# Optimization experiments

Measured on AMD Instinct MI355X. Metric: run time of the kernel, lower is better.

Reference implementation:

```python
import jax, jax.numpy as jnp
import numpy as np

# Detect.__init__ defaults from the source
TOP_K = 5000
CONF_THRESH = 0.01
NMS_THRESH = 0.3
VAR0, VAR1 = 0.1, 0.2   # variance = [0.1, 0.2]
NUM_CLASSES = 2

B = 16
IMAGE = 1280
FMAPS = [320, 160, 80, 40, 20, 10]          # image / steps [4,8,16,32,64,128]
MIN_SIZES = [16, 32, 64, 128, 256, 512]
AR = 1.5                                     # aspect_ratios = [[1.5]] * 6


def make_priors():
    """Vectorized PriorBox.forward: 1 prior per location (max_sizes=[], single AR)."""
    chunks = []
    for f, ms in zip(FMAPS, MIN_SIZES):
        c = (np.arange(f, dtype=np.float32) + 0.5) / f
        cy, cx = np.meshgrid(c, c, indexing='ij')
        s = ms / float(IMAGE)
        w = np.full_like(cx, s / np.sqrt(AR))   # s_k / sqrt(ar)
        h = np.full_like(cx, s * np.sqrt(AR))   # s_k * sqrt(ar)
        chunks.append(np.stack([cx, cy, w, h], -1).reshape(-1, 4))
    pr = np.concatenate(chunks, 0).clip(0.0, 1.0)   # clip=True
    return jnp.asarray(pr, jnp.float32)             # [136500, 4]


def setup_inputs() -> dict:
    key = jax.random.key(0)
    k1, k2 = jax.random.split(key)
    P = sum(f * f for f in FMAPS)   # 136500
    loc_data = 0.5 * jax.random.normal(k1, (B, P, 4), jnp.float32)
    conf_data = jax.random.uniform(k2, (B * P, NUM_CLASSES), jnp.float32)  # post-softmax probs
    prior_data = make_priors()
    return {"loc_data": loc_data, "conf_data": conf_data, "prior_data": prior_data}


def _decode(loc, priors):
    # SSD box decode with variances [0.1, 0.2]; loc, priors: [P,4]
    cxcy = priors[:, :2] + loc[:, :2] * VAR0 * priors[:, 2:]
    wh = priors[:, 2:] * jnp.exp(loc[:, 2:] * VAR1)
    xy1 = cxcy - wh * 0.5
    xy2 = xy1 + wh
    return jnp.concatenate([xy1, xy2], axis=-1)   # [P,4] x1y1x2y2


def _greedy_keep(boxes, valid):
    # Greedy NMS over score-sorted candidates. boxes [K,4], valid [K] bool.
    # Indices/keep decisions are discrete -> computed on stop_gradient'd boxes.
    b = jax.lax.stop_gradient(boxes)
    x1, y1, x2, y2 = b[:, 0], b[:, 1], b[:, 2], b[:, 3]
    area = (x2 - x1) * (y2 - y1)
    idxs = jnp.arange(b.shape[0])

    def body(keep, i):
        iw = jnp.maximum(jnp.minimum(x2, x2[i]) - jnp.maximum(x1, x1[i]), 0.0)
        ih = jnp.maximum(jnp.minimum(y2, y2[i]) - jnp.maximum(y1, y1[i]), 0.0)
        inter = iw * ih
        iou = inter / (area + area[i] - inter)
        suppress = keep[i] & (iou > NMS_THRESH) & (idxs > i)
        return keep & ~suppress, None

    keep, _ = jax.lax.scan(body, valid, idxs)
    return keep


def _detect_one(loc_i, conf_cl, priors):
    # loc_i [P,4]; conf_cl [P] = class-1 scores; returns [TOP_K, 5] (score, x1,y1,x2,y2)
    boxes = _decode(loc_i, priors)
    masked = jnp.where(conf_cl > CONF_THRESH, conf_cl, -1.0)   # c_mask gating
    order = jnp.argsort(-jax.lax.stop_gradient(masked))[:TOP_K]  # scores.sort, top_k cap
    s = masked[order]
    b = boxes[order]
    valid = s > CONF_THRESH
    keep = _greedy_keep(b, valid)
    # scatter kept (score, box) rows, in descending-score order, into dense output
    rank = jnp.cumsum(keep) - 1
    row = jnp.where(keep, rank, TOP_K)            # dropped rows -> scratch slot
    vals = jnp.concatenate([s[:, None], b], axis=1)
    vals = jnp.where(keep[:, None], vals, 0.0)
    out = jnp.zeros((TOP_K + 1, 5), jnp.float32).at[row].set(vals)
    return out[:TOP_K]


def reference(loc_data, conf_data, prior_data):
    num = loc_data.shape[0]
    P = prior_data.shape[0]
    conf_preds = conf_data.reshape(num, P, NUM_CLASSES).transpose(0, 2, 1)  # [B,2,P]
    cls1 = jax.vmap(_detect_one, in_axes=(0, 0, None))(loc_data, conf_preds[:, 1, :], prior_data)
    bg = jnp.zeros_like(cls1)                     # background class row stays zero
    output = jnp.stack([bg, cls1], axis=1)        # [B, 2, TOP_K, 5]
    # NOTE: the original's final `flt[(rank < top_k)...].fill_(0)` fills a boolean-indexed
    # COPY in torch, so it is a no-op on `output`; we faithfully return output unchanged.
    return output
```

## Files before the change

kernel.cpp:

```cpp
#include <hip/hip_runtime.h>
#include <math.h>

#pragma clang fp contract(off)

#define PNUM 136500
#define HPNUM 68250
#define BNUM 16
#define TOPK 5000
#define CAP 8192
#define NB4 4096
#define WBASE 0x2F000u
#define GCS 4
#define NWORDS 79
#define NW32 158
#define GSTRIDE 32
#define CAPE 65536
#define ELDS 14336
#define NXB 128
#define NWC 8
#define NXB2 1024
#define BSTRIDE 5120
#define EBUF 3072
#define SLOTS 4
#define SKI(i) ((i) + ((i) >> 4))

#define OFF_SC    ((size_t)0)
#define OFF_BOX4  (OFF_SC + 320000)
#define OFF_HIST  (OFF_BOX4 + 1280000)
#define OFF_GBCUR (OFF_HIST + 262144)
#define OFF_ECNT  (OFF_GBCUR + 1048576)
#define OFF_BCNT  (OFF_ECNT + 2048)
#define OFF_BCUR  (OFF_BCNT + 65536)
#define OFF_WCNT  (OFF_BCUR + 65536)
#define OFF_ZEND  (OFF_WCNT + 64)
#define OFF_CUT   (OFF_ZEND)
#define OFF_SBASE (OFF_CUT + 64)
#define OFF_WL    (OFF_SBASE + 262144)
#define OFF_KEYS  (OFF_WL + 262144)
#define OFF_EDGE  (OFF_KEYS + 1048576)
#define OFF_GRP   (OFF_EDGE + 4194304)
#define OFF_BOFS  (OFF_GRP)
#define OFF_SIDX  (OFF_GRP + 16384)
#define OFF_SBOX  (OFF_SIDX + 327680)

__device__ __forceinline__ unsigned f2ord(float f) {
    unsigned u = __float_as_uint(f);
    return (u & 0x80000000u) ? ~u : (u | 0x80000000u);
}
__device__ __forceinline__ float ord2f(unsigned o) {
    unsigned u = (o & 0x80000000u) ? (o ^ 0x80000000u) : ~o;
    return __uint_as_float(u);
}
__device__ __forceinline__ int bucketOf(float x) {
    int b = (int)((x + 0.6f) * 71.111115f);
    return (b < 0) ? 0 : ((b > 127) ? 127 : b);
}
__device__ __forceinline__ int rkeyOf(float x1, float x2) {
    int b = bucketOf(x1);
    int wc = bucketOf(x2) - b;
    if (wc > NWC - 1) wc = NWC - 1;
    if (wc < 0) wc = 0;
    return b * NWC + wc;
}

__global__ void __launch_bounds__(512) k_hist(const float* __restrict__ conf,
                                              unsigned* __restrict__ hist) {
    __shared__ unsigned lh[NB4];
    int img = blockIdx.y;
    for (int i = threadIdx.x; i < NB4; i += 512) lh[i] = 0;
    __syncthreads();
    const float4* src = (const float4*)(conf + (size_t)img * PNUM * 2);
    int stride = gridDim.x * 512;
    for (int q = blockIdx.x * 512 + threadIdx.x; q < HPNUM; q += stride) {
        float4 v = src[q];
        if (v.y > 0.01f) atomicAdd(&lh[(f2ord(v.y) >> 14) - WBASE], 1u);
        if (v.w > 0.01f) atomicAdd(&lh[(f2ord(v.w) >> 14) - WBASE], 1u);
    }
    __syncthreads();
    unsigned* h = hist + (size_t)img * NB4;
    for (int i = threadIdx.x; i < NB4; i += 512) {
        unsigned c = lh[i];
        if (c) atomicAdd(&h[i], c);
    }
}

__global__ void __launch_bounds__(256) k_cutoff2(const unsigned* __restrict__ hist,
                                                 unsigned* __restrict__ cut,
                                                 unsigned* __restrict__ sbase,
                                                 unsigned* __restrict__ wl,
                                                 unsigned* __restrict__ wcnt) {
    __shared__ unsigned csum[256], suf[256], scut;
    int img = blockIdx.x;
    int t = threadIdx.x;
    const unsigned* h = hist + (size_t)img * NB4;
    unsigned hv[16];
    unsigned s = 0;
    #pragma unroll
    for (int j = 0; j < 16; ++j) { hv[j] = h[t * 16 + j]; s += hv[j]; }
    csum[t] = s;
    __syncthreads();
    if (t == 0) {
        unsigned a = 0;
        for (int g = 255; g >= 0; --g) { unsigned c = csum[g]; suf[g] = a; a += c; }
        unsigned acc = 0, before = 0;
        int c = -1;
        for (int cc = 255; cc >= 0; --cc) {
            if (acc + csum[cc] >= (unsigned)TOPK) { c = cc; before = acc; break; }
            acc += csum[cc];
        }
        unsigned cutb = WBASE;
        if (c >= 0) {
            unsigned s2 = before;
            cutb = WBASE + (unsigned)c * 16u;
            for (int b = c * 16 + 15; b >= c * 16; --b) {
                s2 += h[b];
                if (s2 >= (unsigned)TOPK) { cutb = WBASE + (unsigned)b; break; }
            }
        }
        scut = cutb;
        cut[img] = cutb;
    }
    __syncthreads();
    unsigned cutb = scut;
    unsigned acc = suf[t];
    unsigned* sb = sbase + (size_t)img * NB4 + t * 16;
    sb[15] = acc;
    #pragma unroll
    for (int j = 14; j >= 0; --j) { acc += hv[j + 1]; sb[j] = acc; }
    #pragma unroll
    for (int j = 0; j < 16; ++j) {
        unsigned b = (unsigned)t * 16u + (unsigned)j;
        if (WBASE + b >= cutb && hv[j] > 0) {
            unsigned x = atomicAdd(wcnt, 1u);
            wl[x] = ((unsigned)img << 12) | b;
        }
    }
}

__global__ void __launch_bounds__(256) k_gather2(
        const float* __restrict__ conf, const unsigned* __restrict__ cut,
        const unsigned* __restrict__ sbase, unsigned* __restrict__ gbcur,
        unsigned long long* __restrict__ keys) {
    int q = blockIdx.x * 256 + threadIdx.x;
    int img = blockIdx.y;
    if (q >= HPNUM) return;
    unsigned cutb = cut[img];
    float4 v = ((const float4*)(conf + (size_t)img * PNUM * 2))[q];
    const unsigned* sb = sbase + (size_t)img * NB4;
    unsigned* gc = gbcur + (size_t)img * NB4 * GCS;
    unsigned long long* kp = keys + (size_t)img * CAP;
    #pragma unroll
    for (int e = 0; e < 2; ++e) {
        float s = e ? v.w : v.y;
        if (s > 0.01f) {
            unsigned o = f2ord(s);
            unsigned w18 = o >> 14;
            if (w18 >= cutb) {
                unsigned wb = w18 - WBASE;
                unsigned pos = sb[wb] + atomicAdd(&gc[wb * GCS], 1u);
                if (pos < (unsigned)CAP)
                    kp[pos] = ((unsigned long long)o << 32)
                              | (unsigned)(~(unsigned)(2 * q + e));
            }
        }
    }
}

__global__ void __launch_bounds__(256) k_ssortdec(
        const unsigned long long* __restrict__ keys,
        const unsigned* __restrict__ hist, const unsigned* __restrict__ sbase,
        const unsigned* __restrict__ wl, const unsigned* __restrict__ wcnt,
        const float* __restrict__ loc, const float* __restrict__ pri,
        float* __restrict__ SC, float4* __restrict__ BOX4,
        unsigned* __restrict__ bcnt) {
    __shared__ unsigned long long sk[1088];
    __shared__ unsigned lhist[NXB2];
    int tid = threadIdx.x;
    unsigned nW = *wcnt;
    for (unsigned w = blockIdx.x; w < nW; w += gridDim.x) {
        unsigned ent = wl[w];
        int img = (int)(ent >> 12);
        int b = (int)(ent & 4095u);
        unsigned cnt = hist[(size_t)img * NB4 + b];
        unsigned base = sbase[(size_t)img * NB4 + b];
        if (base >= (unsigned)TOPK) continue;
        const unsigned long long* kp = keys + (size_t)img * CAP + base;
        for (int i = tid; i < NXB2; i += 256) lhist[i] = 0;
        unsigned scnt = cnt > 1024 ? 1024u : cnt;
        if (scnt >= 2) {
            unsigned np2 = 2;
            while (np2 < scnt) np2 <<= 1;
            for (unsigned i = tid; i < np2; i += 256)
                sk[SKI(i)] = (i < scnt) ? kp[i] : 0ull;
            __syncthreads();
            for (unsigned k = 2; k <= np2; k <<= 1) {
                for (unsigned j = k >> 1; j > 0; j >>= 1) {
                    for (unsigned t = tid; t < (np2 >> 1); t += 256) {
                        unsigned i = ((t & ~(j - 1)) << 1) | (t & (j - 1));
                        unsigned p = i | j;
                        bool desc = ((i & k) == 0);
                        unsigned long long a = sk[SKI(i)], bb = sk[SKI(p)];
                        bool sw = desc ? (a < bb) : (a > bb);
                        if (sw) { sk[SKI(i)] = bb; sk[SKI(p)] = a; }
                    }
                    __syncthreads();
                }
            }
        } else {
            if (tid == 0 && scnt == 1) sk[0] = kp[0];
            __syncthreads();
        }
        size_t ibase = (size_t)img * TOPK;
        for (unsigned i = tid; i < cnt; i += 256) {
            unsigned r = base + i;
            if (r >= (unsigned)TOPK) continue;
            unsigned long long key = (i < scnt) ? sk[SKI(i)] : kp[i];
            float s, x1, y1, x2, y2;
            if (key != 0ull) {
                unsigned ordv = (unsigned)(key >> 32);
                s = ord2f(ordv);
                unsigned p = ~(unsigned)(key & 0xFFFFFFFFull);
                const float* lp = loc + ((size_t)img * PNUM + p) * 4;
                const float* pp = pri + (size_t)p * 4;
                float lx = lp[0], ly = lp[1], lw = lp[2], lh = lp[3];
                float px = pp[0], py = pp[1], pw = pp[2], ph = pp[3];
                float cx = px + (lx * 0.1f) * pw;
                float cy = py + (ly * 0.1f) * ph;
                float w2 = pw * expf(lw * 0.2f);
                float h2 = ph * expf(lh * 0.2f);
                x1 = cx - w2 * 0.5f;
                y1 = cy - h2 * 0.5f;
                x2 = x1 + w2;
                y2 = y1 + h2;
            } else {
                s = -1.0f; x1 = 0.f; y1 = 0.f; x2 = 0.f; y2 = 0.f;
            }
            SC[ibase + r] = s;
            BOX4[ibase + r] = make_float4(x1, y1, x2, y2);
            atomicAdd(&lhist[rkeyOf(x1, x2)], 1u);
        }
        __syncthreads();
        for (int i = tid; i < NXB2; i += 256) {
            unsigned c = lhist[i];
            if (c) atomicAdd(&bcnt[img * NXB2 + i], c);
        }
        __syncthreads();
    }
}

__global__ void __launch_bounds__(256) k_bscat(
        const unsigned* __restrict__ bcnt, unsigned* __restrict__ bcur,
        const float4* __restrict__ BOX4,
        unsigned* __restrict__ bofs, unsigned* __restrict__ sidx,
        float4* __restrict__ sbox, float* __restrict__ out) {
    __shared__ unsigned bpre[NXB2 + 1], tsum[256];
    int img = blockIdx.y;
    int tid = threadIdx.x;
    uint4* oz = (uint4*)(out + (size_t)img * 2 * TOPK * 5);
    uint4 z4 = make_uint4(0u, 0u, 0u, 0u);
    for (int i = blockIdx.x * 256 + tid; i < 12500; i += 20 * 256) oz[i] = z4;
    const unsigned* bc = bcnt + img * NXB2;
    unsigned l0 = bc[tid * 4], l1 = bc[tid * 4 + 1],
             l2 = bc[tid * 4 + 2], l3 = bc[tid * 4 + 3];
    tsum[tid] = l0 + l1 + l2 + l3;
    __syncthreads();
    if (tid == 0) {
        unsigned a = 0;
        for (int t = 0; t < 256; ++t) { unsigned c = tsum[t]; tsum[t] = a; a += c; }
        bpre[NXB2] = a;
    }
    __syncthreads();
    unsigned a = tsum[tid];
    bpre[tid * 4] = a;
    bpre[tid * 4 + 1] = a + l0;
    bpre[tid * 4 + 2] = a + l0 + l1;
    bpre[tid * 4 + 3] = a + l0 + l1 + l2;
    __syncthreads();
    if (blockIdx.x == 0) {
        if (tid < NXB) bofs[img * 130 + tid] = bpre[tid * NWC];
        if (tid == 0) bofs[img * 130 + NXB] = bpre[NXB2];
    }
    int r = blockIdx.x * 256 + tid;
    if (r < TOPK) {
        float4 b = BOX4[(size_t)img * TOPK + r];
        int bk = rkeyOf(b.x, b.z);
        unsigned sp = bpre[bk] + atomicAdd(&bcur[img * NXB2 + bk], 1u);
        int base = img * BSTRIDE;
        sidx[base + sp] = (unsigned)r;
        sbox[base + sp] = b;
    }
}

__global__ void __launch_bounds__(256) k_pair4(
        const unsigned* __restrict__ bofs, const unsigned* __restrict__ sidx,
        const float4* __restrict__ sbox,
        unsigned* __restrict__ ecnt, unsigned* __restrict__ edges) {
    __shared__ unsigned ebuf[EBUF];
    __shared__ unsigned ecl, ebase;
    int img = blockIdx.y;
    int wid = threadIdx.x >> 6;
    int lane = threadIdx.x & 63;
    int sb0 = (blockIdx.x * 4 + wid) * SLOTS;
    if (threadIdx.x == 0) ecl = 0;
    __syncthreads();
    unsigned* ec = ecnt + (size_t)img * GSTRIDE;
    unsigned* eg = edges + (size_t)img * CAPE;
    if (sb0 < TOPK) {
        int base = img * BSTRIDE;
        float x1k[SLOTS], x2k[SLOTS], y1k[SLOTS], y2k[SLOTS], ark[SLOTS];
        unsigned rk[SLOTS];
        bool act[SLOTS];
        #pragma unroll
        for (int k = 0; k < SLOTS; ++k) {
            act[k] = (sb0 + k) < TOPK;
            int s = act[k] ? (sb0 + k) : sb0;
            float4 bk = sbox[base + s];
            x1k[k] = bk.x; y1k[k] = bk.y; x2k[k] = bk.z; y2k[k] = bk.w;
            ark[k] = (bk.z - bk.x) * (bk.w - bk.y);
            rk[k] = sidx[base + s];
        }
        int b1 = bucketOf(x1k[0]);
        int b2m = bucketOf(x2k[0]);
        float gymin = y1k[0], gymax = y2k[0];
        #pragma unroll
        for (int k = 1; k < SLOTS; ++k)
            if (act[k]) {
                int b = bucketOf(x2k[k]); if (b > b2m) b2m = b;
                gymin = fminf(gymin, y1k[k]);
                gymax = fmaxf(gymax, y2k[k]);
            }
        const unsigned* bo = bofs + img * 130;
        unsigned s0 = bo[b1], s1 = bo[b2m + 1];
        if (s0 < s1) {
            unsigned nit = (s1 - s0 + 63) >> 6;
            unsigned c0 = s0 + (unsigned)lane;
            if (c0 > s1 - 1) c0 = s1 - 1;
            float4 cb = sbox[base + c0];
            unsigned cr = sidx[base + c0];
            for (unsigned it = 0; it < nit; ++it) {
                float4 nb = cb; unsigned nr = cr;
                if (it + 1 < nit) {
                    unsigned cn = s0 + (it + 1) * 64 + (unsigned)lane;
                    if (cn > s1 - 1) cn = s1 - 1;
                    nb = sbox[base + cn];
                    nr = sidx[base + cn];
                }
                bool in = (s0 + it * 64 + (unsigned)lane) < s1;
                bool yok = in && (cb.w > gymin) && (cb.y < gymax);
                float bar = (cb.z - cb.x) * (cb.w - cb.y);
                #pragma unroll
                for (int k = 0; k < SLOTS; ++k) {
                    bool hit = false;
                    unsigned edge = 0;
                    if (yok && act[k] && cb.x >= x1k[k]
                        && !(cb.x == x1k[k] && cr <= rk[k])) {
                        float dx = fminf(x2k[k], cb.z) - fmaxf(x1k[k], cb.x);
                        if (dx > 0.0f) {
                            float dy = fminf(y2k[k], cb.w) - fmaxf(y1k[k], cb.y);
                            if (dy > 0.0f) {
                                float inter = dx * dy;
                                float iou = inter / (bar + ark[k] - inter);
                                if (iou > 0.3f) {
                                    unsigned su = (rk[k] < cr) ? rk[k] : cr;
                                    unsigned vi = (rk[k] < cr) ? cr : rk[k];
                                    edge = (vi << 13) | su;
                                    hit = true;
                                }
                            }
                        }
                    }
                    unsigned long long bal = __ballot(hit);
                    if (bal) {
                        int n = __popcll(bal);
                        unsigned wb = 0;
                        if (lane == 0) wb = atomicAdd(&ecl, (unsigned)n);
                        wb = __shfl(wb, 0, 64);
                        if (hit) {
                            unsigned long long lt =
                                (lane == 0) ? 0ull : ((1ull << lane) - 1ull);
                            unsigned p = wb + (unsigned)__popcll(bal & lt);
                            if (p < (unsigned)EBUF) ebuf[p] = edge;
                            else {
                                unsigned gp = atomicAdd(ec, 1u);
                                if (gp < (unsigned)CAPE) eg[gp] = edge;
                            }
                        }
                    }
                }
                cb = nb; cr = nr;
            }
        }
    }
    __syncthreads();
    unsigned n = min(ecl, (unsigned)EBUF);
    if (threadIdx.x == 0 && n) ebase = atomicAdd(ec, n);
    __syncthreads();
    for (unsigned i = threadIdx.x; i < n; i += 256) {
        unsigned p = ebase + i;
        if (p < (unsigned)CAPE) eg[p] = ebuf[i];
    }
}

__global__ void __launch_bounds__(256) k_nms3(
        const float* __restrict__ SC, const float4* __restrict__ BOX4,
        const unsigned* __restrict__ ecnt, const unsigned* __restrict__ edges,
        float* __restrict__ out) {
    __shared__ unsigned lgrp[ELDS];
    __shared__ unsigned undL[160], keptL[160], blockL[160];
    __shared__ unsigned pfx[80];
    __shared__ int chg[2];
    int img = blockIdx.x;
    int tid = threadIdx.x;
    int l = tid & 63;
    int wid = tid >> 6;
    size_t ib = (size_t)img * TOPK;
    const float* sc = SC + ib;

    if (tid < 160) { keptL[tid] = 0u; blockL[tid] = 0u; }
    if (tid < 2) chg[tid] = 0;
    for (int w = wid; w < NWORDS; w += 4) {
        int row = w * 64 + l;
        bool valid = (row < TOPK) && (sc[row] > 0.01f);
        unsigned long long b = __ballot(valid);
        if (l == 0) {
            undL[2 * w]     = (unsigned)b;
            undL[2 * w + 1] = (unsigned)(b >> 32);
        }
    }
    unsigned E = min(ecnt[(size_t)img * GSTRIDE], (unsigned)CAPE);
    const unsigned* eimg = edges + (size_t)img * CAPE;
    bool inl = (E <= (unsigned)ELDS);
    if (inl) for (unsigned e = tid; e < E; e += 256) lgrp[e] = eimg[e];
    __syncthreads();

    for (int round = 0; round < 256; ++round) {
        int par = round & 1;
        for (unsigned e = tid; e < E; e += 256) {
            unsigned ed = inl ? lgrp[e] : eimg[e];
            unsigned s = ed & 8191u;
            unsigned v = ed >> 13;
            unsigned sw = s >> 5, sb = s & 31u;
            unsigned vw = v >> 5, vb = 1u << (v & 31u);
            if ((keptL[sw] >> sb) & 1u) {
                if (undL[vw] & vb) {
                    unsigned old = atomicAnd(&undL[vw], ~vb);
                    if (old & vb) chg[par] = 1;
                }
            } else if ((undL[sw] >> sb) & 1u) {
                if (!(blockL[vw] & vb)) atomicOr(&blockL[vw], vb);
            }
        }
        __syncthreads();
        if (tid < NW32) {
            unsigned nk = undL[tid] & ~blockL[tid];
            if (nk) {
                keptL[tid] |= nk;
                undL[tid] &= ~nk;
                chg[par] = 1;
            }
            blockL[tid] = 0u;
        }
        if (tid == 0) chg[par ^ 1] = 0;
        __syncthreads();
        if (!chg[par]) break;
    }

    if (tid == 0) {
        unsigned acc = 0;
        for (int w = 0; w < NWORDS; ++w) {
            pfx[w] = acc;
            acc += (unsigned)(__popc(keptL[2 * w]) + __popc(keptL[2 * w + 1]));
        }
    }
    __syncthreads();
    const float4* bx = BOX4 + ib;
    float* op = out + (((size_t)img * 2) + 1) * TOPK * 5;
    for (int w = wid; w < NWORDS; w += 4) {
        unsigned long long kw =
            ((unsigned long long)keptL[2 * w + 1] << 32) | keptL[2 * w];
        if (!kw) continue;
        int row = w * 64 + l;
        if ((kw >> l) & 1ull) {
            int rank = (int)pfx[w] + (int)__popcll(kw & ((1ull << l) - 1ull));
            float4 b = bx[row];
            float* r = op + (size_t)rank * 5;
            r[0] = sc[row]; r[1] = b.x; r[2] = b.y; r[3] = b.z; r[4] = b.w;
        }
    }
}

extern "C" void kernel_launch(void* const* d_in, const int* in_sizes, int n_in,
                              void* d_out, int out_size, void* d_ws, size_t ws_size,
                              hipStream_t stream) {
    (void)in_sizes; (void)n_in; (void)ws_size; (void)out_size;
    const float* loc  = (const float*)d_in[0];
    const float* conf = (const float*)d_in[1];
    const float* pri  = (const float*)d_in[2];
    float* out = (float*)d_out;
    char* ws = (char*)d_ws;

    float* SC   = (float*)(ws + OFF_SC);
    float4* BOX4 = (float4*)(ws + OFF_BOX4);
    unsigned* hist = (unsigned*)(ws + OFF_HIST);
    unsigned* cut  = (unsigned*)(ws + OFF_CUT);
    unsigned* sbase = (unsigned*)(ws + OFF_SBASE);
    unsigned* gbcur = (unsigned*)(ws + OFF_GBCUR);
    unsigned long long* keys = (unsigned long long*)(ws + OFF_KEYS);
    unsigned* ecnt = (unsigned*)(ws + OFF_ECNT);
    unsigned* bcnt = (unsigned*)(ws + OFF_BCNT);
    unsigned* bcur = (unsigned*)(ws + OFF_BCUR);
    unsigned* wcnt = (unsigned*)(ws + OFF_WCNT);
    unsigned* wl   = (unsigned*)(ws + OFF_WL);
    unsigned* edges = (unsigned*)(ws + OFF_EDGE);
    unsigned* bofs = (unsigned*)(ws + OFF_BOFS);
    unsigned* sidx = (unsigned*)(ws + OFF_SIDX);
    float4* sbox = (float4*)(ws + OFF_SBOX);

    hipMemsetAsync(ws + OFF_HIST, 0, OFF_ZEND - OFF_HIST, stream);

    dim3 gh1(16, BNUM);
    k_hist<<<gh1, 512, 0, stream>>>(conf, hist);
    k_cutoff2<<<BNUM, 256, 0, stream>>>(hist, cut, sbase, wl, wcnt);
    dim3 gh2((HPNUM + 255) / 256, BNUM);
    k_gather2<<<gh2, 256, 0, stream>>>(conf, cut, sbase, gbcur, keys);
    k_ssortdec<<<1024, 256, 0, stream>>>(keys, hist, sbase, wl, wcnt,
                                         loc, pri, SC, BOX4, bcnt);
    dim3 gb((TOPK + 255) / 256, BNUM);
    k_bscat<<<gb, 256, 0, stream>>>(bcnt, bcur, BOX4, bofs, sidx, sbox, out);
    dim3 pg((TOPK + 4 * SLOTS - 1) / (4 * SLOTS), BNUM);
    k_pair4<<<pg, 256, 0, stream>>>(bofs, sidx, sbox, ecnt, edges);
    k_nms3<<<BNUM, 256, 0, stream>>>(SC, BOX4, ecnt, edges, out);
}
```

Measured before the change: 212.1 us.

## Fuse all detection stages into one cooperative persistent kernel with grid syncs

```diff
diff --git a/kernel.cpp b/kernel.cpp
--- a/kernel.cpp
+++ b/kernel.cpp
@@ -1,7 +1,10 @@
 #include <hip/hip_runtime.h>
+#include <hip/hip_cooperative_groups.h>
 #include <math.h>
 
 #pragma clang fp contract(off)
+
+namespace cg = cooperative_groups;
 
 #define PNUM 136500
 #define HPNUM 68250
@@ -23,6 +26,9 @@
 #define EBUF 3072
 #define SLOTS 4
 #define SKI(i) ((i) + ((i) >> 4))
+#define NVB_G 267
+#define NVB_P 313
+#define NVB_B 20
 
 #define OFF_SC    ((size_t)0)
 #define OFF_BOX4  (OFF_SC + 320000)
@@ -61,6 +67,465 @@
     if (wc > NWC - 1) wc = NWC - 1;
     if (wc < 0) wc = 0;
     return b * NWC + wc;
+}
+
+__global__ void __launch_bounds__(256, 2) k_fused(
+        const float* __restrict__ conf, const float* __restrict__ loc,
+        const float* __restrict__ pri, float* __restrict__ out,
+        char* __restrict__ ws) {
+    float* SC = (float*)(ws + OFF_SC);
+    float4* BOX4 = (float4*)(ws + OFF_BOX4);
+    unsigned* hist = (unsigned*)(ws + OFF_HIST);
+    unsigned* cut = (unsigned*)(ws + OFF_CUT);
+    unsigned* sbase = (unsigned*)(ws + OFF_SBASE);
+    unsigned* gbcur = (unsigned*)(ws + OFF_GBCUR);
+    unsigned long long* keys = (unsigned long long*)(ws + OFF_KEYS);
+    unsigned* ecnt = (unsigned*)(ws + OFF_ECNT);
+    unsigned* bcnt = (unsigned*)(ws + OFF_BCNT);
+    unsigned* bcur = (unsigned*)(ws + OFF_BCUR);
+    unsigned* wcnt = (unsigned*)(ws + OFF_WCNT);
+    unsigned* wl = (unsigned*)(ws + OFF_WL);
+    unsigned* edges = (unsigned*)(ws + OFF_EDGE);
+    unsigned* bofs = (unsigned*)(ws + OFF_BOFS);
+    unsigned* sidx = (unsigned*)(ws + OFF_SIDX);
+    float4* sbox = (float4*)(ws + OFF_SBOX);
+
+    __shared__ unsigned long long smem8[7552];
+    unsigned* su = (unsigned*)smem8;
+    cg::grid_group grid = cg::this_grid();
+    int tid = threadIdx.x;
+    int nB = (int)gridDim.x;
+
+    {
+        unsigned* z = (unsigned*)(ws + OFF_HIST);
+        size_t nz = (OFF_ZEND - OFF_HIST) / 4;
+        for (size_t i = (size_t)blockIdx.x * 256 + tid; i < nz;
+             i += (size_t)nB * 256) z[i] = 0;
+    }
+    grid.sync();
+
+    {
+        unsigned* lh = su;
+        for (int v = blockIdx.x; v < 32 * BNUM; v += nB) {
+            int img = v >> 5, sl = v & 31;
+            for (int i = tid; i < NB4; i += 256) lh[i] = 0;
+            __syncthreads();
+            const float4* src = (const float4*)(conf + (size_t)img * PNUM * 2);
+            for (int q = sl * 256 + tid; q < HPNUM; q += 32 * 256) {
+                float4 vv = src[q];
+                if (vv.y > 0.01f) atomicAdd(&lh[(f2ord(vv.y) >> 14) - WBASE], 1u);
+                if (vv.w > 0.01f) atomicAdd(&lh[(f2ord(vv.w) >> 14) - WBASE], 1u);
+            }
+            __syncthreads();
+            unsigned* h = hist + (size_t)img * NB4;
+            for (int i = tid; i < NB4; i += 256) {
+                unsigned c = lh[i];
+                if (c) atomicAdd(&h[i], c);
+            }
+            __syncthreads();
+        }
+    }
+    grid.sync();
+
+    {
+        unsigned* csum = su;
+        unsigned* suf = su + 256;
+        unsigned* scut = su + 512;
+        for (int img = blockIdx.x; img < BNUM; img += nB) {
+            int t = tid;
+            const unsigned* h = hist + (size_t)img * NB4;
+            unsigned hv[16];
+            unsigned s = 0;
+            #pragma unroll
+            for (int j = 0; j < 16; ++j) { hv[j] = h[t * 16 + j]; s += hv[j]; }
+            csum[t] = s;
+            __syncthreads();
+            if (t == 0) {
+                unsigned a = 0;
+                for (int g = 255; g >= 0; --g) { unsigned c = csum[g]; suf[g] = a; a += c; }
+                unsigned acc = 0, before = 0;
+                int c = -1;
+                for (int cc = 255; cc >= 0; --cc) {
+                    if (acc + csum[cc] >= (unsigned)TOPK) { c = cc; before = acc; break; }
+                    acc += csum[cc];
+                }
+                unsigned cutb = WBASE;
+                if (c >= 0) {
+                    unsigned s2 = before;
+                    cutb = WBASE + (unsigned)c * 16u;
+                    for (int b = c * 16 + 15; b >= c * 16; --b) {
+                        s2 += h[b];
+                        if (s2 >= (unsigned)TOPK) { cutb = WBASE + (unsigned)b; break; }
+                    }
+                }
+                scut[0] = cutb;
+                cut[img] = cutb;
+            }
+            __syncthreads();
+            unsigned cutb = scut[0];
+            unsigned acc = suf[t];
+            unsigned* sb = sbase + (size_t)img * NB4 + t * 16;
+            sb[15] = acc;
+            #pragma unroll
+            for (int j = 14; j >= 0; --j) { acc += hv[j + 1]; sb[j] = acc; }
+            #pragma unroll
+            for (int j = 0; j < 16; ++j) {
+                unsigned b = (unsigned)t * 16u + (unsigned)j;
+                if (WBASE + b >= cutb && hv[j] > 0) {
+                    unsigned x = atomicAdd(wcnt, 1u);
+                    wl[x] = ((unsigned)img << 12) | b;
+                }
+            }
+            __syncthreads();
+        }
+    }
+    grid.sync();
+
+    for (int v = blockIdx.x; v < NVB_G * BNUM; v += nB) {
+        int img = v / NVB_G;
+        int q = (v - img * NVB_G) * 256 + tid;
+        if (q < HPNUM) {
+            unsigned cutb = cut[img];
+            float4 vv = ((const float4*)(conf + (size_t)img * PNUM * 2))[q];
+            const unsigned* sb = sbase + (size_t)img * NB4;
+            unsigned* gc = gbcur + (size_t)img * NB4 * GCS;
+            unsigned long long* kp = keys + (size_t)img * CAP;
+            #pragma unroll
+            for (int e = 0; e < 2; ++e) {
+                float s = e ? vv.w : vv.y;
+                if (s > 0.01f) {
+                    unsigned o = f2ord(s);
+                    unsigned w18 = o >> 14;
+                    if (w18 >= cutb) {
+                        unsigned wb = w18 - WBASE;
+                        unsigned pos = sb[wb] + atomicAdd(&gc[wb * GCS], 1u);
+                        if (pos < (unsigned)CAP)
+                            kp[pos] = ((unsigned long long)o << 32)
+                                      | (unsigned)(~(unsigned)(2 * q + e));
+                    }
+                }
+            }
+        }
+    }
+    grid.sync();
+
+    {
+        unsigned long long* sk = smem8;
+        unsigned* lhist = (unsigned*)(smem8 + 1088);
+        unsigned nW = *wcnt;
+        for (unsigned w = blockIdx.x; w < nW; w += nB) {
+            unsigned ent = wl[w];
+            int img = (int)(ent >> 12);
+            int b = (int)(ent & 4095u);
+            unsigned cnt = hist[(size_t)img * NB4 + b];
+            unsigned base = sbase[(size_t)img * NB4 + b];
+            if (base >= (unsigned)TOPK) continue;
+            const unsigned long long* kp = keys + (size_t)img * CAP + base;
+            for (int i = tid; i < NXB2; i += 256) lhist[i] = 0;
+            unsigned scnt = cnt > 1024 ? 1024u : cnt;
+            if (scnt >= 2) {
+                unsigned np2 = 2;
+                while (np2 < scnt) np2 <<= 1;
+                for (unsigned i = tid; i < np2; i += 256)
+                    sk[SKI(i)] = (i < scnt) ? kp[i] : 0ull;
+                __syncthreads();
+                for (unsigned k = 2; k <= np2; k <<= 1) {
+                    for (unsigned j = k >> 1; j > 0; j >>= 1) {
+                        for (unsigned t = tid; t < (np2 >> 1); t += 256) {
+                            unsigned i = ((t & ~(j - 1)) << 1) | (t & (j - 1));
+                            unsigned p = i | j;
+                            bool desc = ((i & k) == 0);
+                            unsigned long long a = sk[SKI(i)], bb = sk[SKI(p)];
+                            bool sw = desc ? (a < bb) : (a > bb);
+                            if (sw) { sk[SKI(i)] = bb; sk[SKI(p)] = a; }
+                        }
+                        __syncthreads();
+                    }
+                }
+            } else {
+                if (tid == 0 && scnt == 1) sk[0] = kp[0];
+                __syncthreads();
+            }
+            size_t ibase = (size_t)img * TOPK;
+            for (unsigned i = tid; i < cnt; i += 256) {
+                unsigned r = base + i;
+                if (r >= (unsigned)TOPK) continue;
+                unsigned long long key = (i < scnt) ? sk[SKI(i)] : kp[i];
+                float s, x1, y1, x2, y2;
+                if (key != 0ull) {
+                    unsigned ordv = (unsigned)(key >> 32);
+                    s = ord2f(ordv);
+                    unsigned p = ~(unsigned)(key & 0xFFFFFFFFull);
+                    const float* lp = loc + ((size_t)img * PNUM + p) * 4;
+                    const float* pp = pri + (size_t)p * 4;
+                    float lx = lp[0], ly = lp[1], lw = lp[2], lh2 = lp[3];
+                    float px = pp[0], py = pp[1], pw = pp[2], ph = pp[3];
+                    float cx = px + (lx * 0.1f) * pw;
+                    float cy = py + (ly * 0.1f) * ph;
+                    float w2 = pw * expf(lw * 0.2f);
+                    float h2 = ph * expf(lh2 * 0.2f);
+                    x1 = cx - w2 * 0.5f;
+                    y1 = cy - h2 * 0.5f;
+                    x2 = x1 + w2;
+                    y2 = y1 + h2;
+                } else {
+                    s = -1.0f; x1 = 0.f; y1 = 0.f; x2 = 0.f; y2 = 0.f;
+                }
+                SC[ibase + r] = s;
+                BOX4[ibase + r] = make_float4(x1, y1, x2, y2);
+                atomicAdd(&lhist[rkeyOf(x1, x2)], 1u);
+            }
+            __syncthreads();
+            for (int i = tid; i < NXB2; i += 256) {
+                unsigned c = lhist[i];
+                if (c) atomicAdd(&bcnt[img * NXB2 + i], c);
+            }
+            __syncthreads();
+        }
+    }
+    grid.sync();
+
+    {
+        unsigned* bpre = su;
+        unsigned* tsum = su + 1032;
+        for (int v = blockIdx.x; v < NVB_B * BNUM; v += nB) {
+            int img = v / NVB_B;
+            int bx = v - img * NVB_B;
+            uint4* oz = (uint4*)(out + (size_t)img * 2 * TOPK * 5);
+            uint4 z4 = make_uint4(0u, 0u, 0u, 0u);
+            for (int i = bx * 256 + tid; i < 12500; i += NVB_B * 256) oz[i] = z4;
+            const unsigned* bc = bcnt + img * NXB2;
+            unsigned l0 = bc[tid * 4], l1 = bc[tid * 4 + 1],
+                     l2 = bc[tid * 4 + 2], l3 = bc[tid * 4 + 3];
+            tsum[tid] = l0 + l1 + l2 + l3;
+            __syncthreads();
+            if (tid == 0) {
+                unsigned a = 0;
+                for (int t = 0; t < 256; ++t) { unsigned c = tsum[t]; tsum[t] = a; a += c; }
+                bpre[NXB2] = a;
+            }
+            __syncthreads();
+            unsigned a = tsum[tid];
+            bpre[tid * 4] = a;
+            bpre[tid * 4 + 1] = a + l0;
+            bpre[tid * 4 + 2] = a + l0 + l1;
+            bpre[tid * 4 + 3] = a + l0 + l1 + l2;
+            __syncthreads();
+            if (bx == 0) {
+                if (tid < NXB) bofs[img * 130 + tid] = bpre[tid * NWC];
+                if (tid == 0) bofs[img * 130 + NXB] = bpre[NXB2];
+            }
+            int r = bx * 256 + tid;
+            if (r < TOPK) {
+                float4 b = BOX4[(size_t)img * TOPK + r];
+                int bk = rkeyOf(b.x, b.z);
+                unsigned sp = bpre[bk] + atomicAdd(&bcur[img * NXB2 + bk], 1u);
+                int base = img * BSTRIDE;
+                sidx[base + sp] = (unsigned)r;
+                sbox[base + sp] = b;
+            }
+            __syncthreads();
+        }
+    }
+    grid.sync();
+
+    {
+        unsigned* ebuf = su;
+        unsigned* ecl = su + EBUF;
+        unsigned* ebase = su + EBUF + 1;
+        int wid = tid >> 6;
+        int lane = tid & 63;
+        for (int v = blockIdx.x; v < NVB_P * BNUM; v += nB) {
+            int img = v / NVB_P;
+            int bxx = v - img * NVB_P;
+            if (tid == 0) ecl[0] = 0;
+            __syncthreads();
+            unsigned* ec = ecnt + (size_t)img * GSTRIDE;
+            unsigned* eg = edges + (size_t)img * CAPE;
+            int sb0 = (bxx * 4 + wid) * SLOTS;
+            if (sb0 < TOPK) {
+                int base = img * BSTRIDE;
+                float x1k[SLOTS], x2k[SLOTS], y1k[SLOTS], y2k[SLOTS], ark[SLOTS];
+                unsigned rk[SLOTS];
+                bool act[SLOTS];
+                #pragma unroll
+                for (int k = 0; k < SLOTS; ++k) {
+                    act[k] = (sb0 + k) < TOPK;
+                    int s = act[k] ? (sb0 + k) : sb0;
+                    float4 bk = sbox[base + s];
+                    x1k[k] = bk.x; y1k[k] = bk.y; x2k[k] = bk.z; y2k[k] = bk.w;
+                    ark[k] = (bk.z - bk.x) * (bk.w - bk.y);
+                    rk[k] = sidx[base + s];
+                }
+                int b1 = bucketOf(x1k[0]);
+                int b2m = bucketOf(x2k[0]);
+                float gymin = y1k[0], gymax = y2k[0];
+                #pragma unroll
+                for (int k = 1; k < SLOTS; ++k)
+                    if (act[k]) {
+                        int b = bucketOf(x2k[k]); if (b > b2m) b2m = b;
+                        gymin = fminf(gymin, y1k[k]);
+                        gymax = fmaxf(gymax, y2k[k]);
+                    }
+                const unsigned* bo = bofs + img * 130;
+                unsigned s0 = bo[b1], s1 = bo[b2m + 1];
+                if (s0 < s1) {
+                    unsigned nit = (s1 - s0 + 63) >> 6;
+                    unsigned c0 = s0 + (unsigned)lane;
+                    if (c0 > s1 - 1) c0 = s1 - 1;
+                    float4 cb = sbox[base + c0];
+                    unsigned cr = sidx[base + c0];
+                    for (unsigned it = 0; it < nit; ++it) {
+                        float4 nb = cb; unsigned nr = cr;
+                        if (it + 1 < nit) {
+                            unsigned cn = s0 + (it + 1) * 64 + (unsigned)lane;
+                            if (cn > s1 - 1) cn = s1 - 1;
+                            nb = sbox[base + cn];
+                            nr = sidx[base + cn];
+                        }
+                        bool in = (s0 + it * 64 + (unsigned)lane) < s1;
+                        bool yok = in && (cb.w > gymin) && (cb.y < gymax);
+                        float bar = (cb.z - cb.x) * (cb.w - cb.y);
+                        #pragma unroll
+                        for (int k = 0; k < SLOTS; ++k) {
+                            bool hit = false;
+                            unsigned edge = 0;
+                            if (yok && act[k] && cb.x >= x1k[k]
+                                && !(cb.x == x1k[k] && cr <= rk[k])) {
+                                float dx = fminf(x2k[k], cb.z) - fmaxf(x1k[k], cb.x);
+                                if (dx > 0.0f) {
+                                    float dy = fminf(y2k[k], cb.w) - fmaxf(y1k[k], cb.y);
+                                    if (dy > 0.0f) {
+                                        float inter = dx * dy;
+                                        float iou = inter / (bar + ark[k] - inter);
+                                        if (iou > 0.3f) {
+                                            unsigned sm = (rk[k] < cr) ? rk[k] : cr;
+                                            unsigned vi = (rk[k] < cr) ? cr : rk[k];
+                                            edge = (vi << 13) | sm;
+                                            hit = true;
+                                        }
+                                    }
+                                }
+                            }
+                            unsigned long long bal = __ballot(hit);
+                            if (bal) {
+                                int n = __popcll(bal);
+                                unsigned wb = 0;
+                                if (lane == 0) wb = atomicAdd(ecl, (unsigned)n);
+                                wb = __shfl(wb, 0, 64);
+                                if (hit) {
+                                    unsigned long long lt =
+                                        (lane == 0) ? 0ull : ((1ull << lane) - 1ull);
+                                    unsigned p = wb + (unsigned)__popcll(bal & lt);
+                                    if (p < (unsigned)EBUF) ebuf[p] = edge;
+                                    else {
+                                        unsigned gp = atomicAdd(ec, 1u);
+                                        if (gp < (unsigned)CAPE) eg[gp] = edge;
+                                    }
+                                }
+                            }
+                        }
+                        cb = nb; cr = nr;
+                    }
+                }
+            }
+            __syncthreads();
+            unsigned n = min(ecl[0], (unsigned)EBUF);
+            if (tid == 0 && n) ebase[0] = atomicAdd(ec, n);
+            __syncthreads();
+            for (unsigned i = tid; i < n; i += 256) {
+                unsigned p = ebase[0] + i;
+                if (p < (unsigned)CAPE) eg[p] = ebuf[i];
+            }
+            __syncthreads();
+        }
+    }
+    grid.sync();
+
+    {
+        unsigned* lgrp = su;
+        unsigned* undL = su + ELDS;
+        unsigned* keptL = undL + 160;
+        unsigned* blockL = keptL + 160;
+        unsigned* pfx = blockL + 160;
+        int* chg = (int*)(pfx + 80);
+        int l = tid & 63;
+        int wid = tid >> 6;
+        for (int img = blockIdx.x; img < BNUM; img += nB) {
+            size_t ib = (size_t)img * TOPK;
+            const float* sc = SC + ib;
+            if (tid < 160) { keptL[tid] = 0u; blockL[tid] = 0u; }
+            if (tid < 2) chg[tid] = 0;
+            for (int w = wid; w < NWORDS; w += 4) {
+                int row = w * 64 + l;
+                bool valid = (row < TOPK) && (sc[row] > 0.01f);
+                unsigned long long b = __ballot(valid);
+                if (l == 0) {
+                    undL[2 * w] = (unsigned)b;
+                    undL[2 * w + 1] = (unsigned)(b >> 32);
+                }
+            }
+            unsigned E = min(ecnt[(size_t)img * GSTRIDE], (unsigned)CAPE);
+            const unsigned* eimg = edges + (size_t)img * CAPE;
+            bool inl = (E <= (unsigned)ELDS);
+            if (inl) for (unsigned e = tid; e < E; e += 256) lgrp[e] = eimg[e];
+            __syncthreads();
+            for (int round = 0; round < 256; ++round) {
+                int par = round & 1;
+                for (unsigned e = tid; e < E; e += 256) {
+                    unsigned ed = inl ? lgrp[e] : eimg[e];
+                    unsigned s = ed & 8191u;
+                    unsigned vv = ed >> 13;
+                    unsigned sw = s >> 5, sb = s & 31u;
+                    unsigned vw = vv >> 5, vb = 1u << (vv & 31u);
+                    if ((keptL[sw] >> sb) & 1u) {
+                        if (undL[vw] & vb) {
+                            unsigned old = atomicAnd(&undL[vw], ~vb);
+                            if (old & vb) chg[par] = 1;
+                        }
+                    } else if ((undL[sw] >> sb) & 1u) {
+                        if (!(blockL[vw] & vb)) atomicOr(&blockL[vw], vb);
+                    }
+                }
+                __syncthreads();
+                if (tid < NW32) {
+                    unsigned nk = undL[tid] & ~blockL[tid];
+                    if (nk) {
+                        keptL[tid] |= nk;
+                        undL[tid] &= ~nk;
+                        chg[par] = 1;
+                    }
+                    blockL[tid] = 0u;
+                }
+                if (tid == 0) chg[par ^ 1] = 0;
+                __syncthreads();
+                if (!chg[par]) break;
+            }
+            if (tid == 0) {
+                unsigned acc = 0;
+                for (int w = 0; w < NWORDS; ++w) {
+                    pfx[w] = acc;
+                    acc += (unsigned)(__popc(keptL[2 * w]) + __popc(keptL[2 * w + 1]));
+                }
+            }
+            __syncthreads();
+            const float4* bx = BOX4 + ib;
+            float* op = out + (((size_t)img * 2) + 1) * TOPK * 5;
+            for (int w = wid; w < NWORDS; w += 4) {
+                unsigned long long kw =
+                    ((unsigned long long)keptL[2 * w + 1] << 32) | keptL[2 * w];
+                if (!kw) continue;
+                int row = w * 64 + l;
+                if ((kw >> l) & 1ull) {
+                    int rank = (int)pfx[w] + (int)__popcll(kw & ((1ull << l) - 1ull));
+                    float4 b = bx[row];
+                    float* r = op + (size_t)rank * 5;
+                    r[0] = sc[row]; r[1] = b.x; r[2] = b.y; r[3] = b.z; r[4] = b.w;
+                }
+            }
+            __syncthreads();
+        }
+    }
 }
 
 __global__ void __launch_bounds__(512) k_hist(const float* __restrict__ conf,
@@ -222,12 +687,12 @@
                 unsigned p = ~(unsigned)(key & 0xFFFFFFFFull);
                 const float* lp = loc + ((size_t)img * PNUM + p) * 4;
                 const float* pp = pri + (size_t)p * 4;
-                float lx = lp[0], ly = lp[1], lw = lp[2], lh = lp[3];
+                float lx = lp[0], ly = lp[1], lw = lp[2], lh2 = lp[3];
                 float px = pp[0], py = pp[1], pw = pp[2], ph = pp[3];
                 float cx = px + (lx * 0.1f) * pw;
                 float cy = py + (ly * 0.1f) * ph;
                 float w2 = pw * expf(lw * 0.2f);
-                float h2 = ph * expf(lh * 0.2f);
+                float h2 = ph * expf(lh2 * 0.2f);
                 x1 = cx - w2 * 0.5f;
                 y1 = cy - h2 * 0.5f;
                 x2 = x1 + w2;
@@ -415,7 +880,6 @@
     int wid = tid >> 6;
     size_t ib = (size_t)img * TOPK;
     const float* sc = SC + ib;
-
     if (tid < 160) { keptL[tid] = 0u; blockL[tid] = 0u; }
     if (tid < 2) chg[tid] = 0;
     for (int w = wid; w < NWORDS; w += 4) {
@@ -423,7 +887,7 @@
         bool valid = (row < TOPK) && (sc[row] > 0.01f);
         unsigned long long b = __ballot(valid);
         if (l == 0) {
-            undL[2 * w]     = (unsigned)b;
+            undL[2 * w] = (unsigned)b;
             undL[2 * w + 1] = (unsigned)(b >> 32);
         }
     }
@@ -432,7 +896,6 @@
     bool inl = (E <= (unsigned)ELDS);
     if (inl) for (unsigned e = tid; e < E; e += 256) lgrp[e] = eimg[e];
     __syncthreads();
-
     for (int round = 0; round < 256; ++round) {
         int par = round & 1;
         for (unsigned e = tid; e < E; e += 256) {
@@ -464,7 +927,6 @@
         __syncthreads();
         if (!chg[par]) break;
     }
-
     if (tid == 0) {
         unsigned acc = 0;
         for (int w = 0; w < NWORDS; ++w) {
@@ -493,41 +955,59 @@
                               void* d_out, int out_size, void* d_ws, size_t ws_size,
                               hipStream_t stream) {
     (void)in_sizes; (void)n_in; (void)ws_size; (void)out_size;
-    const float* loc  = (const float*)d_in[0];
+    const float* conf_loc = (const float*)d_in[0];
     const float* conf = (const float*)d_in[1];
-    const float* pri  = (const float*)d_in[2];
+    const float* pri = (const float*)d_in[2];
+    const float* loc = conf_loc;
     float* out = (float*)d_out;
     char* ws = (char*)d_ws;
 
-    float* SC   = (float*)(ws + OFF_SC);
-    float4* BOX4 = (float4*)(ws + OFF_BOX4);
-    unsigned* hist = (unsigned*)(ws + OFF_HIST);
-    unsigned* cut  = (unsigned*)(ws + OFF_CUT);
-    unsigned* sbase = (unsigned*)(ws + OFF_SBASE);
-    unsigned* gbcur = (unsigned*)(ws + OFF_GBCUR);
-    unsigned long long* keys = (unsigned long long*)(ws + OFF_KEYS);
-    unsigned* ecnt = (unsigned*)(ws + OFF_ECNT);
-    unsigned* bcnt = (unsigned*)(ws + OFF_BCNT);
-    unsigned* bcur = (unsigned*)(ws + OFF_BCUR);
-    unsigned* wcnt = (unsigned*)(ws + OFF_WCNT);
-    unsigned* wl   = (unsigned*)(ws + OFF_WL);
-    unsigned* edges = (unsigned*)(ws + OFF_EDGE);
-    unsigned* bofs = (unsigned*)(ws + OFF_BOFS);
-    unsigned* sidx = (unsigned*)(ws + OFF_SIDX);
-    float4* sbox = (float4*)(ws + OFF_SBOX);
-
-    hipMemsetAsync(ws + OFF_HIST, 0, OFF_ZEND - OFF_HIST, stream);
-
-    dim3 gh1(16, BNUM);
-    k_hist<<<gh1, 512, 0, stream>>>(conf, hist);
-    k_cutoff2<<<BNUM, 256, 0, stream>>>(hist, cut, sbase, wl, wcnt);
-    dim3 gh2((HPNUM + 255) / 256, BNUM);
-    k_gather2<<<gh2, 256, 0, stream>>>(conf, cut, sbase, gbcur, keys);
-    k_ssortdec<<<1024, 256, 0, stream>>>(keys, hist, sbase, wl, wcnt,
-                                         loc, pri, SC, BOX4, bcnt);
-    dim3 gb((TOPK + 255) / 256, BNUM);
-    k_bscat<<<gb, 256, 0, stream>>>(bcnt, bcur, BOX4, bofs, sidx, sbox, out);
-    dim3 pg((TOPK + 4 * SLOTS - 1) / (4 * SLOTS), BNUM);
-    k_pair4<<<pg, 256, 0, stream>>>(bofs, sidx, sbox, ecnt, edges);
-    k_nms3<<<BNUM, 256, 0, stream>>>(SC, BOX4, ecnt, edges, out);
-}
+    static int s_grid = -1;
+    if (s_grid < 0) {
+        int nb = 0;
+        if (hipOccupancyMaxActiveBlocksPerMultiprocessor(&nb, k_fused, 256, 0)
+                != hipSuccess || nb < 1) nb = 1;
+        int g = nb * 256;
+        if (g > 512) g = 512;
+        if (g < 16) g = 16;
+        s_grid = g;
+    }
+
+    void* kargs[] = { (void*)&conf, (void*)&loc, (void*)&pri,
+                      (void*)&out, (void*)&ws };
+    hipError_t err = hipLaunchCooperativeKernel(
+        k_fused, dim3(s_grid), dim3(256), kargs, 0, stream);
+
+    if (err != hipSuccess) {
+        float* SC = (float*)(ws + OFF_SC);
+        float4* BOX4 = (float4*)(ws + OFF_BOX4);
+        unsigned* hist = (unsigned*)(ws + OFF_HIST);
+        unsigned* cut = (unsigned*)(ws + OFF_CUT);
+        unsigned* sbase = (unsigned*)(ws + OFF_SBASE);
+        unsigned* gbcur = (unsigned*)(ws + OFF_GBCUR);
+        unsigned long long* keys = (unsigned long long*)(ws + OFF_KEYS);
+        unsigned* ecnt = (unsigned*)(ws + OFF_ECNT);
+        unsigned* bcnt = (unsigned*)(ws + OFF_BCNT);
+        unsigned* bcur = (unsigned*)(ws + OFF_BCUR);
+        unsigned* wcnt = (unsigned*)(ws + OFF_WCNT);
+        unsigned* wl = (unsigned*)(ws + OFF_WL);
+        unsigned* edges = (unsigned*)(ws + OFF_EDGE);
+        unsigned* bofs = (unsigned*)(ws + OFF_BOFS);
+        unsigned* sidx = (unsigned*)(ws + OFF_SIDX);
+        float4* sbox = (float4*)(ws + OFF_SBOX);
+
+        hipMemsetAsync(ws + OFF_HIST, 0, OFF_ZEND - OFF_HIST, stream);
+        dim3 gh1(16, BNUM);
+        k_hist<<<gh1, 512, 0, stream>>>(conf, hist);
+        k_cutoff2<<<BNUM, 256, 0, stream>>>(hist, cut, sbase, wl, wcnt);
+        dim3 gh2((HPNUM + 255) / 256, BNUM);
+        k_gather2<<<gh2, 256, 0, stream>>>(conf, cut, sbase, gbcur, keys);
+        k_ssortdec<<<1024, 256, 0, stream>>>(keys, hist, sbase, wl, wcnt,
+                                             loc, pri, SC, BOX4, bcnt);
+        dim3 gb((TOPK + 255) / 256, BNUM);
+        k_bscat<<<gb, 256, 0, stream>>>(bcnt, bcur, BOX4, bofs, sidx, sbox, out);
+        dim3 pg((TOPK + 4 * SLOTS - 1) / (4 * SLOTS), BNUM);
+        k_pair4<<<pg, 256, 0, stream>>>(bofs, sidx, sbox, ecnt, edges);
+        k_nms3<<<BNUM, 256, 0, stream>>>(SC, BOX4, ecnt, edges, out);
+    }
+}
```

New measurement: 645.8 us. +204.5%, slower.
